# Kernel optimization log

Hardware: AMD Instinct MI355X
Metric: run time of the kernel (lower is better)

## Reference

```python
import jax, jax.numpy as jnp
import numpy as np
from jax.scipy.special import digamma

# Dims (see init_kwargs): pose P=4 -> D=16, stem A=128, primary caps B=32,
# classes C=10, class-caps kernel K=6 (== primary feature map size), 3 routing iters.
P, D, A, B, C, K, ITER = 4, 16, 128, 32, 10, 6, 3
N = B * K * K                                    # input capsules routed to each class capsule
ALPHA0, KAPPA0, NU0 = 1.0, 1.0, float(D + 1)     # Dirichlet/Normal-Wishart priors (m0=0, Psi0=I, cov='diag')
BN_EPS, EPS = 1e-5, 1e-8


def conv2d(x, w, s):
    return jax.lax.conv_general_dilated(x, w, (s, s), 'VALID',
                                        dimension_numbers=('NCHW', 'OIHW', 'NCHW'))


def bn(x, gamma, beta, axes):
    # batch-norm with batch statistics (training-mode math)
    mu = x.mean(axes, keepdims=True)
    var = x.var(axes, keepdims=True)
    return (x - mu) * jax.lax.rsqrt(var + BN_EPS) * gamma + beta


def setup_inputs():
    key = jax.random.key(0)
    ks = jax.random.split(key, 4)
    f32 = jnp.float32
    x = jax.random.normal(ks[0], (128, 3, 32, 32), dtype=f32)
    conv1_w = jax.random.normal(ks[1], (A, 3, 5, 5), dtype=f32) * 0.1
    bn1_g = jnp.ones((A,), f32); bn1_b = jnp.zeros((A,), f32)
    prim_w = jax.random.normal(ks[2], (B * D + B, A, 3, 3), dtype=f32) * 0.05
    bna_g = jnp.ones((B,), f32); bna_b = jnp.zeros((B,), f32)
    bnp_g = jnp.ones((B,), f32); bnp_b = jnp.zeros((B,), f32)
    W_ij = jax.random.normal(ks[3], (B, C, K, K, P, P), dtype=f32) * 0.3
    return dict(x=x, conv1_w=conv1_w, bn1_g=bn1_g, bn1_b=bn1_b, prim_w=prim_w,
                bna_g=bna_g, bna_b=bna_b, bnp_g=bnp_g, bnp_b=bnp_b, W_ij=W_ij)


def _vb_stats(Ra, V):
    # Ra: (b,N,C) responsibility * input activation; V: (b,N,C,D) votes
    Nj = Ra.sum(1) + EPS                                         # (b,C)
    xbar = jnp.einsum('bnc,bncd->bcd', Ra, V) / Nj[..., None]    # weighted vote mean
    diff = V - xbar[:, None]
    sigma = jnp.einsum('bnc,bncd->bcd', Ra, diff * diff) / Nj[..., None]  # diag cov
    kappa = KAPPA0 + Nj
    m = Nj[..., None] * xbar / kappa[..., None]                  # posterior mean (m0 = 0)
    nu = NU0 + Nj
    Psi = 1.0 + Nj[..., None] * sigma + (KAPPA0 * Nj / kappa)[..., None] * xbar * xbar  # Psi0 = I (diag)
    return Nj, kappa, m, nu, Psi


def _expectations(Nj, nu, Psi, d_idx):
    alpha = ALPHA0 + Nj
    E_lnpi = digamma(alpha) - digamma(alpha.sum(-1, keepdims=True))
    E_lnLam = (digamma(0.5 * (nu[..., None] + 1.0 - d_idx)).sum(-1)
               + D * jnp.log(2.0) - jnp.log(Psi).sum(-1))
    return E_lnpi, E_lnLam


def reference(x, conv1_w, bn1_g, bn1_b, prim_w, bna_g, bna_b, bnp_g, bnp_b, W_ij):
    b = x.shape[0]
    # --- stem: Conv5x5/s2 + BN + ReLU ---
    h = conv2d(x, conv1_w, 2)                                    # (b,A,14,14)
    h = jax.nn.relu(bn(h, bn1_g[None, :, None, None], bn1_b[None, :, None, None], (0, 2, 3)))
    # --- primary capsules: Conv3x3/s2 -> poses + activations ---
    pc = conv2d(h, prim_w, 2)                                    # (b,B*D+B,6,6)
    poses, a = pc[:, :B * D], pc[:, B * D:]
    a = jax.nn.sigmoid(bn(a, bna_g[None, :, None, None], bna_b[None, :, None, None], (0, 2, 3)))
    poses = bn(poses.reshape(b, B, D, K, K),
               bnp_g[None, :, None, None, None], bnp_b[None, :, None, None, None], (0, 2, 3, 4))
    poses = poses.reshape(b, B, P, P, K, K)
    # --- class capsules: votes V = W_ij @ pose, kernel covers whole 6x6 map ---
    V = jnp.einsum('icxypq,biqrxy->bicxypr', W_ij, poses)        # (b,B,C,K,K,P,P)
    V = V.transpose(0, 1, 3, 4, 2, 5, 6).reshape(b, N, C, D)
    a_i = a.reshape(b, N)
    # --- variational Bayes routing (diag Normal-Wishart, ITER iterations) ---
    d_idx = jnp.arange(1, D + 1, dtype=x.dtype)
    R = jnp.full((b, N, C), 1.0 / C, dtype=x.dtype)
    for t in range(ITER):
        Nj, kappa, m, nu, Psi = _vb_stats(R * a_i[:, :, None], V)
        if t < ITER - 1:
            E_lnpi, E_lnLam = _expectations(Nj, nu, Psi, d_idx)
            dm = V - m[:, None]
            quad = D / kappa[:, None, :] + nu[:, None, :] * jnp.einsum('bncd,bcd->bnc', dm * dm, 1.0 / Psi)
            lnp = (E_lnpi[:, None] + 0.5 * E_lnLam[:, None]
                   - 0.5 * D * jnp.log(2.0 * jnp.pi) - 0.5 * quad)
            R = jax.nn.softmax(lnp, axis=-1)
    E_lnpi, E_lnLam = _expectations(Nj, nu, Psi, d_idx)
    logits = E_lnpi + 0.5 * E_lnLam                              # (b,C)
    yhat = jax.nn.sigmoid(bn(logits, 1.0, 0.0, (0,)))            # BatchNorm1d(affine=False)
    return yhat
```

## Files before the change

### kernel.cpp

```cpp
#include <hip/hip_runtime.h>
#include <hip/hip_bf16.h>

#define NB 128
#define AA 128
#define BB 32
#define CC 10
#define KK 6
#define DD 16
#define NN 1152
#define H1 14
#define CH2 544
#define NG 4608
#define KG 1152
#define MG 576

typedef short bfrag8 __attribute__((ext_vector_type(8)));
typedef float facc4 __attribute__((ext_vector_type(4)));

__device__ __forceinline__ unsigned short f2bf(float f) {
    unsigned u = __float_as_uint(f);
    u += 0x7FFF + ((u >> 16) & 1);
    return (unsigned short)(u >> 16);
}
__device__ __forceinline__ float bf2f(unsigned short s) {
    return __uint_as_float(((unsigned)s) << 16);
}

__global__ __launch_bounds__(256, 3) void k_conv1(const float* __restrict__ x,
                                                  const float* __restrict__ w,
                                                  float* __restrict__ h) {
    __shared__ __align__(16) float sX[3][7][32];
    __shared__ float sWf[AA * 75];
    const int p = blockIdx.x;
    const int b = blockIdx.y;
    const int tid = threadIdx.x;
    for (int j = tid; j < AA * 75; j += 256) sWf[j] = w[j];
    for (int j = tid; j < 3 * 7 * 32; j += 256) {
        int col = j & 31; int t2 = j >> 5; int row = t2 % 7; int ic = t2 / 7;
        sX[ic][row][col] = x[b * 3072 + ic * 1024 + (4 * p + row) * 32 + col];
    }
    __syncthreads();
    const int oc = tid & 127, ry = tid >> 7;
    const int r = 2 * p + ry;
    float acc[14];
#pragma unroll
    for (int j = 0; j < 14; ++j) acc[j] = 0.f;
    const float* wr = sWf + oc * 75;
#pragma unroll
    for (int ic = 0; ic < 3; ++ic) {
#pragma unroll
        for (int ky = 0; ky < 5; ++ky) {
            const float* xr = &sX[ic][2 * ry + ky][0];
            float row[32];
#pragma unroll
            for (int q = 0; q < 8; ++q) {
                float4 v = *reinterpret_cast<const float4*>(xr + q * 4);
                row[q * 4 + 0] = v.x; row[q * 4 + 1] = v.y;
                row[q * 4 + 2] = v.z; row[q * 4 + 3] = v.w;
            }
            float w0 = wr[ic * 25 + ky * 5 + 0];
            float w1 = wr[ic * 25 + ky * 5 + 1];
            float w2 = wr[ic * 25 + ky * 5 + 2];
            float w3 = wr[ic * 25 + ky * 5 + 3];
            float w4 = wr[ic * 25 + ky * 5 + 4];
#pragma unroll
            for (int ox = 0; ox < 14; ++ox) {
                float s = acc[ox];
                s = fmaf(row[2 * ox + 0], w0, s);
                s = fmaf(row[2 * ox + 1], w1, s);
                s = fmaf(row[2 * ox + 2], w2, s);
                s = fmaf(row[2 * ox + 3], w3, s);
                s = fmaf(row[2 * ox + 4], w4, s);
                acc[ox] = s;
            }
        }
    }
    float* out = h + ((size_t)(b * AA + oc) * 14 + r) * 14;
#pragma unroll
    for (int q = 0; q < 7; ++q)
        *reinterpret_cast<float2*>(out + q * 2) = make_float2(acc[q * 2], acc[q * 2 + 1]);
}

__device__ __forceinline__ void blk_reduce2(float& s, float& s2, int tid) {
#pragma unroll
    for (int o = 32; o > 0; o >>= 1) { s += __shfl_down(s, o); s2 += __shfl_down(s2, o); }
    __shared__ float ls[4], lq[4];
    int lane = tid & 63, wid = tid >> 6;
    if (lane == 0) { ls[wid] = s; lq[wid] = s2; }
    __syncthreads();
    if (tid == 0) {
        s = ls[0] + ls[1] + ls[2] + ls[3];
        s2 = lq[0] + lq[1] + lq[2] + lq[3];
    }
}

__global__ void k_bnstats1a(const float* __restrict__ h, float* __restrict__ part) {
    int c = blockIdx.x & 127, sl = blockIdx.x >> 7;
    int tid = threadIdx.x;
    float s = 0.f, s2 = 0.f;
    for (int j = tid; j < 16 * 196; j += 256) {
        int b = sl * 16 + j / 196, hw = j % 196;
        float v = h[((size_t)b * AA + c) * 196 + hw];
        s += v; s2 += v * v;
    }
    blk_reduce2(s, s2, tid);
    if (tid == 0) { part[c * 8 + sl] = s; part[1024 + c * 8 + sl] = s2; }
}

__global__ void k_pim(const float* __restrict__ w, const float* __restrict__ h,
                      const float* __restrict__ part1,
                      const float* __restrict__ bn1_g, const float* __restrict__ bn1_b,
                      unsigned short* __restrict__ Ah, unsigned short* __restrict__ Al,
                      unsigned short* __restrict__ Bh, unsigned short* __restrict__ Bl) {
    const int blk = blockIdx.x;
    const int tid = threadIdx.x;
    if (blk < 324) {
        int t = blk * 256 + tid;
        int row = t / (KG / 8), seg = t % (KG / 8);
        alignas(16) unsigned short hi[8], lo[8];
        if (row < CH2) {
            const float* src = w + (size_t)row * KG + seg * 8;
#pragma unroll
            for (int j = 0; j < 8; ++j) {
                float v = src[j];
                unsigned short hh = f2bf(v);
                hi[j] = hh;
                lo[j] = f2bf(v - bf2f(hh));
            }
        } else {
#pragma unroll
            for (int j = 0; j < 8; ++j) { hi[j] = 0; lo[j] = 0; }
        }
        *reinterpret_cast<uint4*>(Ah + (size_t)row * KG + seg * 8) = *reinterpret_cast<const uint4*>(hi);
        *reinterpret_cast<uint4*>(Al + (size_t)row * KG + seg * 8) = *reinterpret_cast<const uint4*>(lo);
        return;
    }
    __shared__ float sBn1[2 * AA];
    if (tid < AA) {
        int c = tid;
        float s = 0.f, s2 = 0.f;
#pragma unroll
        for (int sl = 0; sl < 8; ++sl) { s += part1[c * 8 + sl]; s2 += part1[1024 + c * 8 + sl]; }
        const float n = (float)(NB * 196);
        float mu = s / n;
        float var = s2 / n - mu * mu;
        float sc = bn1_g[c] * rsqrtf(var + 1e-5f);
        sBn1[c] = sc;
        sBn1[AA + c] = bn1_b[c] - mu * sc;
    }
    __syncthreads();
    int t = (blk - 324) * 256 + tid;
    int n = t / (KG / 8), seg = t % (KG / 8);
    int b = n / 36, xy = n % 36;
    int oy = xy / 6, ox = xy % 6;
    const float* hb = h + (size_t)b * (AA * 196) + (2 * oy) * 14 + 2 * ox;
    alignas(16) unsigned short hi[8], lo[8];
#pragma unroll
    for (int j = 0; j < 8; ++j) {
        int k = seg * 8 + j;
        int ic = k / 9, kk = k - ic * 9;
        int ky = kk / 3, kx = kk - ky * 3;
        float v = hb[ic * 196 + ky * 14 + kx];
        v = fmaxf(fmaf(v, sBn1[ic], sBn1[AA + ic]), 0.f);
        unsigned short hh = f2bf(v);
        hi[j] = hh;
        lo[j] = f2bf(v - bf2f(hh));
    }
    *reinterpret_cast<uint4*>(Bh + (size_t)n * KG + seg * 8) = *reinterpret_cast<const uint4*>(hi);
    *reinterpret_cast<uint4*>(Bl + (size_t)n * KG + seg * 8) = *reinterpret_cast<const uint4*>(lo);
}

__global__ __launch_bounds__(256, 4) void k_gemm(const unsigned short* __restrict__ Ah,
                                                 const unsigned short* __restrict__ Al,
                                                 const unsigned short* __restrict__ Bh,
                                                 const unsigned short* __restrict__ Bl,
                                                 float* __restrict__ pcT) {
    __shared__ alignas(16) unsigned short sAh[64][44], sAl[64][44];
    __shared__ alignas(16) unsigned short sBh[64][44], sBl[64][44];
    const int s = blockIdx.x;
    const int k8 = s & 7, j = s >> 3;
    const int jm = j / 9;
    const int y = k8 + 8 * jm;
    const int xg = j - 9 * jm;
    const int oc0 = xg * 64;
    const int n0 = y * 64;
    const int tid = threadIdx.x;
    const int lane = tid & 63, wv = tid >> 6;
    const int wm = wv >> 1, wn = wv & 1;
    const int quad = lane >> 4, r16 = lane & 15;
    const int srow = tid >> 2, sseg = tid & 3;

    facc4 acc[2][2] = {};
    const size_t gA = (size_t)(oc0 + srow) * KG + sseg * 8;
    const size_t gB = (size_t)(n0 + srow) * KG + sseg * 8;

    uint4 vAh = *reinterpret_cast<const uint4*>(Ah + gA);
    uint4 vAl = *reinterpret_cast<const uint4*>(Al + gA);
    uint4 vBh = *reinterpret_cast<const uint4*>(Bh + gB);
    uint4 vBl = *reinterpret_cast<const uint4*>(Bl + gB);

    for (int ks = 0; ks < KG / 32; ++ks) {
        __syncthreads();
        *reinterpret_cast<uint4*>(&sAh[srow][sseg * 8]) = vAh;
        *reinterpret_cast<uint4*>(&sAl[srow][sseg * 8]) = vAl;
        *reinterpret_cast<uint4*>(&sBh[srow][sseg * 8]) = vBh;
        *reinterpret_cast<uint4*>(&sBl[srow][sseg * 8]) = vBl;
        __syncthreads();
        if (ks + 1 < KG / 32) {
            const int k0n = (ks + 1) * 32;
            vAh = *reinterpret_cast<const uint4*>(Ah + gA + k0n);
            vAl = *reinterpret_cast<const uint4*>(Al + gA + k0n);
            vBh = *reinterpret_cast<const uint4*>(Bh + gB + k0n);
            vBl = *reinterpret_cast<const uint4*>(Bl + gB + k0n);
        }
        bfrag8 ah[2], al[2], bh[2], bl[2];
#pragma unroll
        for (int i = 0; i < 2; ++i) {
            ah[i] = *reinterpret_cast<const bfrag8*>(&sAh[wm * 32 + i * 16 + r16][quad * 8]);
            al[i] = *reinterpret_cast<const bfrag8*>(&sAl[wm * 32 + i * 16 + r16][quad * 8]);
            bh[i] = *reinterpret_cast<const bfrag8*>(&sBh[wn * 32 + i * 16 + r16][quad * 8]);
            bl[i] = *reinterpret_cast<const bfrag8*>(&sBl[wn * 32 + i * 16 + r16][quad * 8]);
        }
#pragma unroll
        for (int i = 0; i < 2; ++i)
#pragma unroll
            for (int jj = 0; jj < 2; ++jj) {
                acc[i][jj] = __builtin_amdgcn_mfma_f32_16x16x32_bf16(ah[i], bh[jj], acc[i][jj], 0, 0, 0);
                acc[i][jj] = __builtin_amdgcn_mfma_f32_16x16x32_bf16(ah[i], bl[jj], acc[i][jj], 0, 0, 0);
                acc[i][jj] = __builtin_amdgcn_mfma_f32_16x16x32_bf16(al[i], bh[jj], acc[i][jj], 0, 0, 0);
            }
    }
#pragma unroll
    for (int i = 0; i < 2; ++i) {
        int oc_base = oc0 + wm * 32 + i * 16 + quad * 4;
        if (oc_base >= CH2) continue;
#pragma unroll
        for (int jj = 0; jj < 2; ++jj) {
            int n = n0 + wn * 32 + jj * 16 + r16;
            *reinterpret_cast<facc4*>(pcT + (size_t)n * CH2 + oc_base) = acc[i][jj];
        }
    }
}

__global__ void k_bnstats2a(const float* __restrict__ pcT, float* __restrict__ part) {
    int blk = blockIdx.x, tid = threadIdx.x;
    float s = 0.f, s2 = 0.f;
    if (blk < 256) {
        int i = blk >> 3, sl = blk & 7;
        for (int j = tid; j < 576 * 4; j += 256) {
            int row = sl * 576 + (j >> 2), q = j & 3;
            float4 v = *reinterpret_cast<const float4*>(pcT + (size_t)row * CH2 + i * 16 + q * 4);
            s += v.x + v.y + v.z + v.w;
            s2 += v.x * v.x + v.y * v.y + v.z * v.z + v.w * v.w;
        }
        blk_reduce2(s, s2, tid);
        if (tid == 0) { part[blk] = s; part[256 + blk] = s2; }
    } else {
        int t2 = blk - 256;
        int ch = t2 >> 1, sl = t2 & 1;
        for (int j = tid; j < 2304; j += 256) {
            int row = sl * 2304 + j;
            float v = pcT[(size_t)row * CH2 + BB * DD + ch];
            s += v; s2 += v * v;
        }
        blk_reduce2(s, s2, tid);
        if (tid == 0) { part[512 + t2] = s; part[576 + t2] = s2; }
    }
}

__device__ __forceinline__ float digammaf_(float x) {
    float r = 0.f;
    while (x < 6.f) { r -= 1.f / x; x += 1.f; }
    float xi = 1.f / x;
    float xi2 = xi * xi;
    return r + logf(x) - 0.5f * xi -
           xi2 * (0.0833333333f - xi2 * (0.0083333333f - xi2 * 0.0039682540f));
}

template <int FIRST>
__global__ __launch_bounds__(640) void k_routed(
    const float* __restrict__ pcT, const float* __restrict__ part2,
    const float* __restrict__ bna_g, const float* __restrict__ bna_b,
    const float* __restrict__ bnp_g, const float* __restrict__ bnp_b,
    const float* __restrict__ Wij,
    const float* __restrict__ S0i, const float* __restrict__ S1i, const float* __restrict__ S2i,
    float* __restrict__ S0o, float* __restrict__ S1o, float* __restrict__ S2o) {
    const int b = blockIdx.x >> 1, half = blockIdx.x & 1;
    const int tid = threadIdx.x;
    const int c = tid >> 6, lane = tid & 63;
    __shared__ float sLnp[CC][66];
    __shared__ float sBn2[128];
    __shared__ __align__(16) float sP[64][20];
    __shared__ float sA[64];
    __shared__ float sM[CC][16], sGq[CC][16], sBase[CC];
    if (tid < 64) {
        if (tid < 32) {
            float s = 0.f, s2 = 0.f;
#pragma unroll
            for (int sl = 0; sl < 8; ++sl) { s += part2[tid * 8 + sl]; s2 += part2[256 + tid * 8 + sl]; }
            const float n = (float)(NB * DD * 36);
            float mu = s / n, var = s2 / n - mu * mu;
            float sc = bnp_g[tid] * rsqrtf(var + 1e-5f);
            sBn2[tid] = sc; sBn2[32 + tid] = bnp_b[tid] - mu * sc;
        } else {
            int ch = tid - 32;
            float s = part2[512 + ch * 2] + part2[512 + ch * 2 + 1];
            float s2 = part2[576 + ch * 2] + part2[576 + ch * 2 + 1];
            const float n = (float)(NB * 36);
            float mu = s / n, var = s2 / n - mu * mu;
            float sc = bna_g[ch] * rsqrtf(var + 1e-5f);
            sBn2[64 + ch] = sc; sBn2[96 + ch] = bna_b[ch] - mu * sc;
        }
    }
    if (!FIRST && tid < 160) {
        int cc = tid >> 4, d = tid & 15;
        int bc = b * CC + cc;
        float njraw = S0i[bc] + S0i[NB * CC + bc];
        float nj = njraw + 1e-8f;
        float kappa = 1.f + nj;
        float nu = 17.f + nj;
        float s1 = S1i[bc * 16 + d] + S1i[(NB * CC + bc) * 16 + d];
        float s2v = S2i[bc * 16 + d] + S2i[(NB * CC + bc) * 16 + d];
        float xbar = s1 / nj;
        float sig = (s2v - 2.f * xbar * s1 + xbar * xbar * njraw) / nj;
        float Psi = 1.f + nj * sig + (nj / kappa) * xbar * xbar;
        sM[cc][d] = nj * xbar / kappa;
        sGq[cc][d] = 0.5f * nu / Psi;
        float term = digammaf_(0.5f * (nu + 1.f - (float)(d + 1))) - logf(Psi);
#pragma unroll
        for (int o = 8; o > 0; o >>= 1) term += __shfl_down(term, o, 16);
        if (d == 0) {
            float asum = 0.f;
#pragma unroll
            for (int k = 0; k < CC; ++k)
                asum += 1.f + S0i[b * CC + k] + S0i[NB * CC + b * CC + k] + 1e-8f;
            float elnlam = 16.f * 0.69314718056f + term;
            float elnpi = digammaf_(1.f + nj) - digammaf_(asum);
            float lb = elnpi + 0.5f * elnlam;
            sBase[cc] = lb - 8.f * 1.83787706641f - 8.f / kappa;
        }
    }
    __syncthreads();
    float mc[16], Gc[16], basec = 0.f;
    if (!FIRST) {
#pragma unroll
        for (int d = 0; d < 16; ++d) { mc[d] = sM[c][d]; Gc[d] = sGq[c][d]; }
        basec = sBase[c];
    }
    float s0 = 0.f, s1[16], s2[16];
#pragma unroll
    for (int d = 0; d < 16; ++d) { s1[d] = 0.f; s2[d] = 0.f; }

#pragma unroll 1
    for (int it = 0; it < 9; ++it) {
        if (tid < 256) {
            int r = tid >> 2, q = tid & 3;
            int n = half * 576 + it * 64 + r;
            int i = n / 36, xy = n - i * 36;
            int row = b * 36 + xy;
            float4 v = *reinterpret_cast<const float4*>(pcT + (size_t)row * CH2 + i * 16 + q * 4);
            float psc = sBn2[i], psh = sBn2[32 + i];
            v.x = fmaf(v.x, psc, psh); v.y = fmaf(v.y, psc, psh);
            v.z = fmaf(v.z, psc, psh); v.w = fmaf(v.w, psc, psh);
            *reinterpret_cast<float4*>(&sP[r][q * 4]) = v;
        } else if (tid < 320) {
            int r = tid - 256;
            int n = half * 576 + it * 64 + r;
            int i = n / 36, xy = n - i * 36;
            int row = b * 36 + xy;
            float va = fmaf(pcT[(size_t)row * CH2 + BB * DD + i], sBn2[64 + i], sBn2[96 + i]);
            sA[r] = 1.f / (1.f + expf(-va));
        }
        __syncthreads();
        const int n = half * 576 + it * 64 + lane;
        const int i = n / 36, xy = n - i * 36;
        const float4* wp = reinterpret_cast<const float4*>(Wij + (((size_t)i * CC + c) * 36 + xy) * 16);
        alignas(16) float P[16], W[16];
        *reinterpret_cast<float4*>(&P[0])  = *reinterpret_cast<const float4*>(&sP[lane][0]);
        *reinterpret_cast<float4*>(&P[4])  = *reinterpret_cast<const float4*>(&sP[lane][4]);
        *reinterpret_cast<float4*>(&P[8])  = *reinterpret_cast<const float4*>(&sP[lane][8]);
        *reinterpret_cast<float4*>(&P[12]) = *reinterpret_cast<const float4*>(&sP[lane][12]);
        *reinterpret_cast<float4*>(&W[0])  = wp[0];
        *reinterpret_cast<float4*>(&W[4])  = wp[1];
        *reinterpret_cast<float4*>(&W[8])  = wp[2];
        *reinterpret_cast<float4*>(&W[12]) = wp[3];
        float V[16];
#pragma unroll
        for (int p = 0; p < 4; ++p)
#pragma unroll
            for (int r = 0; r < 4; ++r)
                V[p * 4 + r] = W[p * 4 + 0] * P[0 + r] + W[p * 4 + 1] * P[4 + r] +
                               W[p * 4 + 2] * P[8 + r] + W[p * 4 + 3] * P[12 + r];
        float av = sA[lane];
        float wgt;
        if (FIRST) {
            wgt = 0.1f * av;
            __syncthreads();
        } else {
            float q = 0.f;
#pragma unroll
            for (int d = 0; d < 16; ++d) {
                float dm = V[d] - mc[d];
                q = fmaf(dm * dm, Gc[d], q);
            }
            float lnp = basec - q;
            sLnp[c][lane] = lnp;
            __syncthreads();
            float mx = -1e30f;
#pragma unroll
            for (int cc = 0; cc < CC; ++cc) mx = fmaxf(mx, sLnp[cc][lane]);
            float ssum = 0.f;
#pragma unroll
            for (int cc = 0; cc < CC; ++cc) ssum += expf(sLnp[cc][lane] - mx);
            wgt = expf(lnp - mx) / ssum * av;
        }
        s0 += wgt;
#pragma unroll
        for (int d = 0; d < 16; ++d) {
            float wv = wgt * V[d];
            s1[d] += wv;
            s2[d] = fmaf(wv, V[d], s2[d]);
        }
    }
#pragma unroll
    for (int o = 32; o > 0; o >>= 1) {
        s0 += __shfl_down(s0, o);
#pragma unroll
        for (int k = 0; k < 16; ++k) {
            s1[k] += __shfl_down(s1[k], o);
            s2[k] += __shfl_down(s2[k], o);
        }
    }
    if (lane == 0) {
        int idx = half * (NB * CC) + b * CC + c;
        S0o[idx] = s0;
#pragma unroll
        for (int k = 0; k < 16; ++k) { S1o[idx * 16 + k] = s1[k]; S2o[idx * 16 + k] = s2[k]; }
    }
}

__global__ void k_expect_final(const float* __restrict__ S0p, const float* __restrict__ S1p,
                               const float* __restrict__ S2p, float* __restrict__ logits) {
    int b = blockIdx.x;
    int c = threadIdx.x;
    __shared__ float alph[CC];
    float njraw = 0.f;
    if (c < CC) {
        njraw = S0p[b * CC + c] + S0p[NB * CC + b * CC + c];
        alph[c] = 1.f + njraw + 1e-8f;
    }
    __syncthreads();
    if (c < CC) {
        int bc = b * CC + c;
        float nj = njraw + 1e-8f;
        float asum = 0.f;
#pragma unroll
        for (int k = 0; k < CC; ++k) asum += alph[k];
        float kappa = 1.f + nj;
        float nu = 17.f + nj;
        float S0 = njraw;
        float elnlam = 16.f * 0.69314718056f;
        for (int d = 0; d < 16; ++d) {
            float s1 = S1p[bc * 16 + d] + S1p[(NB * CC + bc) * 16 + d];
            float s2v = S2p[bc * 16 + d] + S2p[(NB * CC + bc) * 16 + d];
            float xbar = s1 / nj;
            float sig = (s2v - 2.f * xbar * s1 + xbar * xbar * S0) / nj;
            float Psi = 1.f + nj * sig + (nj / kappa) * xbar * xbar;
            elnlam += digammaf_(0.5f * (nu + 1.f - (float)(d + 1))) - logf(Psi);
        }
        float elnpi = digammaf_(1.f + nj) - digammaf_(asum);
        logits[bc] = elnpi + 0.5f * elnlam;
    }
}

__global__ void k_final(const float* __restrict__ logits, float* __restrict__ out) {
    int c = blockIdx.x;
    int b = threadIdx.x;
    float v = logits[b * CC + c];
    float s = v, s2 = v * v;
#pragma unroll
    for (int o = 32; o > 0; o >>= 1) { s += __shfl_down(s, o); s2 += __shfl_down(s2, o); }
    __shared__ float ls[2], lq[2];
    int lane = b & 63, wid = b >> 6;
    if (lane == 0) { ls[wid] = s; lq[wid] = s2; }
    __syncthreads();
    float mu = (ls[0] + ls[1]) * (1.f / 128.f);
    float var = (lq[0] + lq[1]) * (1.f / 128.f) - mu * mu;
    out[b * CC + c] = 1.f / (1.f + expf(-(v - mu) * rsqrtf(var + 1e-5f)));
}

extern "C" void kernel_launch(void* const* d_in, const int* in_sizes, int n_in,
                              void* d_out, int out_size, void* d_ws, size_t ws_size,
                              hipStream_t stream) {
    (void)in_sizes; (void)n_in; (void)out_size; (void)ws_size;
    const float* x       = (const float*)d_in[0];
    const float* conv1_w = (const float*)d_in[1];
    const float* bn1_g   = (const float*)d_in[2];
    const float* bn1_b   = (const float*)d_in[3];
    const float* prim_w  = (const float*)d_in[4];
    const float* bna_g   = (const float*)d_in[5];
    const float* bna_b   = (const float*)d_in[6];
    const float* bnp_g   = (const float*)d_in[7];
    const float* bnp_b   = (const float*)d_in[8];
    const float* Wij     = (const float*)d_in[9];

    float* ws = (float*)d_ws;
    float* h   = ws;
    float* pcT = ws + 3211264;
    unsigned short* Bh = (unsigned short*)(ws + 5718016);
    unsigned short* Bl = (unsigned short*)(ws + 8372224);
    unsigned short* Ahp = (unsigned short*)(ws + 11026432);
    unsigned short* Alp = (unsigned short*)(ws + 11358208);
    float* S0a    = ws + 11690368;
    float* S1a    = ws + 11692928;
    float* S2a    = ws + 11733888;
    float* S0b    = ws + 11774848;
    float* S1b    = ws + 11777408;
    float* S2b    = ws + 11818368;
    float* logits = ws + 11859328;
    float* part1  = ws + 11860608;
    float* part2  = ws + 11862656;
    float* out    = (float*)d_out;

    k_conv1<<<dim3(7, 128), 256, 0, stream>>>(x, conv1_w, h);
    k_bnstats1a<<<1024, 256, 0, stream>>>(h, part1);
    k_pim<<<2916, 256, 0, stream>>>(prim_w, h, part1, bn1_g, bn1_b, Ahp, Alp, Bh, Bl);
    k_gemm<<<648, 256, 0, stream>>>(Ahp, Alp, Bh, Bl, pcT);
    k_bnstats2a<<<320, 256, 0, stream>>>(pcT, part2);

    k_routed<1><<<256, 640, 0, stream>>>(pcT, part2, bna_g, bna_b, bnp_g, bnp_b, Wij,
                                         S0a, S1a, S2a, S0a, S1a, S2a);
    k_routed<0><<<256, 640, 0, stream>>>(pcT, part2, bna_g, bna_b, bnp_g, bnp_b, Wij,
                                         S0a, S1a, S2a, S0b, S1b, S2b);
    k_routed<0><<<256, 640, 0, stream>>>(pcT, part2, bna_g, bna_b, bnp_g, bnp_b, Wij,
                                         S0b, S1b, S2b, S0a, S1a, S2a);
    k_expect_final<<<128, 64, 0, stream>>>(S0a, S1a, S2a, logits);

    k_final<<<10, 128, 0, stream>>>(logits, out);
}
```

Baseline: 178.2 us.

## Fuse batch-norm statistics into conv1 and GEMM epilogues, merge final kernels

Conv1 now emits per-block channel sums and sums of squares, and a small reduction kernel turns them into BN1 scale and shift. This replaces a separate full pass over the conv1 output. The GEMM epilogue computes the BN2 partial statistics from its accumulators, which removes the separate stats kernel that re-read pcT. The expectation and final sigmoid kernels are merged into one. Together this removes two launches and about two full re-reads of intermediates, at the cost of extra shuffles and syncs in the epilogues and more partial-sum entries for the routed kernel to reduce.

```diff
diff --git a/kernel.cpp b/kernel.cpp
--- a/kernel.cpp
+++ b/kernel.cpp
@@ -28,9 +28,12 @@
 
 __global__ __launch_bounds__(256, 3) void k_conv1(const float* __restrict__ x,
                                                   const float* __restrict__ w,
-                                                  float* __restrict__ h) {
+                                                  float* __restrict__ h,
+                                                  float* __restrict__ part1s,
+                                                  float* __restrict__ part1q) {
     __shared__ __align__(16) float sX[3][7][32];
     __shared__ float sWf[AA * 75];
+    __shared__ float sS[128], sQ[128];
     const int p = blockIdx.x;
     const int b = blockIdx.y;
     const int tid = threadIdx.x;
@@ -79,6 +82,16 @@
 #pragma unroll
     for (int q = 0; q < 7; ++q)
         *reinterpret_cast<float2*>(out + q * 2) = make_float2(acc[q * 2], acc[q * 2 + 1]);
+    float s_th = 0.f, q_th = 0.f;
+#pragma unroll
+    for (int ox = 0; ox < 14; ++ox) { s_th += acc[ox]; q_th = fmaf(acc[ox], acc[ox], q_th); }
+    if (ry == 1) { sS[oc] = s_th; sQ[oc] = q_th; }
+    __syncthreads();
+    if (ry == 0) {
+        int blk = p * 128 + b;
+        part1s[oc * 896 + blk] = s_th + sS[oc];
+        part1q[oc * 896 + blk] = q_th + sQ[oc];
+    }
 }
 
 __device__ __forceinline__ void blk_reduce2(float& s, float& s2, int tid) {
@@ -94,22 +107,26 @@
     }
 }
 
-__global__ void k_bnstats1a(const float* __restrict__ h, float* __restrict__ part) {
-    int c = blockIdx.x & 127, sl = blockIdx.x >> 7;
+__global__ void k_bnred1(const float* __restrict__ part1s, const float* __restrict__ part1q,
+                         const float* __restrict__ g, const float* __restrict__ be,
+                         float* __restrict__ bn1) {
+    int c = blockIdx.x;
     int tid = threadIdx.x;
     float s = 0.f, s2 = 0.f;
-    for (int j = tid; j < 16 * 196; j += 256) {
-        int b = sl * 16 + j / 196, hw = j % 196;
-        float v = h[((size_t)b * AA + c) * 196 + hw];
-        s += v; s2 += v * v;
-    }
+    for (int j = tid; j < 896; j += 256) { s += part1s[c * 896 + j]; s2 += part1q[c * 896 + j]; }
     blk_reduce2(s, s2, tid);
-    if (tid == 0) { part[c * 8 + sl] = s; part[1024 + c * 8 + sl] = s2; }
+    if (tid == 0) {
+        const float n = (float)(NB * 196);
+        float mu = s / n;
+        float var = s2 / n - mu * mu;
+        float sc = g[c] * rsqrtf(var + 1e-5f);
+        bn1[c] = sc;
+        bn1[AA + c] = be[c] - mu * sc;
+    }
 }
 
 __global__ void k_pim(const float* __restrict__ w, const float* __restrict__ h,
-                      const float* __restrict__ part1,
-                      const float* __restrict__ bn1_g, const float* __restrict__ bn1_b,
+                      const float* __restrict__ bn1,
                       unsigned short* __restrict__ Ah, unsigned short* __restrict__ Al,
                       unsigned short* __restrict__ Bh, unsigned short* __restrict__ Bl) {
     const int blk = blockIdx.x;
@@ -136,18 +153,7 @@
         return;
     }
     __shared__ float sBn1[2 * AA];
-    if (tid < AA) {
-        int c = tid;
-        float s = 0.f, s2 = 0.f;
-#pragma unroll
-        for (int sl = 0; sl < 8; ++sl) { s += part1[c * 8 + sl]; s2 += part1[1024 + c * 8 + sl]; }
-        const float n = (float)(NB * 196);
-        float mu = s / n;
-        float var = s2 / n - mu * mu;
-        float sc = bn1_g[c] * rsqrtf(var + 1e-5f);
-        sBn1[c] = sc;
-        sBn1[AA + c] = bn1_b[c] - mu * sc;
-    }
+    sBn1[tid] = bn1[tid];
     __syncthreads();
     int t = (blk - 324) * 256 + tid;
     int n = t / (KG / 8), seg = t % (KG / 8);
@@ -174,9 +180,11 @@
                                                  const unsigned short* __restrict__ Al,
                                                  const unsigned short* __restrict__ Bh,
                                                  const unsigned short* __restrict__ Bl,
-                                                 float* __restrict__ pcT) {
+                                                 float* __restrict__ pcT,
+                                                 float* __restrict__ part2) {
     __shared__ alignas(16) unsigned short sAh[64][44], sAl[64][44];
     __shared__ alignas(16) unsigned short sBh[64][44], sBl[64][44];
+    __shared__ float sRed[128];
     const int s = blockIdx.x;
     const int k8 = s & 7, j = s >> 3;
     const int jm = j / 9;
@@ -240,31 +248,63 @@
             *reinterpret_cast<facc4*>(pcT + (size_t)n * CH2 + oc_base) = acc[i][jj];
         }
     }
-}
-
-__global__ void k_bnstats2a(const float* __restrict__ pcT, float* __restrict__ part) {
-    int blk = blockIdx.x, tid = threadIdx.x;
-    float s = 0.f, s2 = 0.f;
-    if (blk < 256) {
-        int i = blk >> 3, sl = blk & 7;
-        for (int j = tid; j < 576 * 4; j += 256) {
-            int row = sl * 576 + (j >> 2), q = j & 3;
-            float4 v = *reinterpret_cast<const float4*>(pcT + (size_t)row * CH2 + i * 16 + q * 4);
-            s += v.x + v.y + v.z + v.w;
-            s2 += v.x * v.x + v.y * v.y + v.z * v.z + v.w * v.w;
-        }
-        blk_reduce2(s, s2, tid);
-        if (tid == 0) { part[blk] = s; part[256 + blk] = s2; }
+    if (xg < 8) {
+        float ps[2], pq[2];
+#pragma unroll
+        for (int i = 0; i < 2; ++i) {
+            float sv = 0.f, qv = 0.f;
+#pragma unroll
+            for (int jj = 0; jj < 2; ++jj)
+#pragma unroll
+                for (int comp = 0; comp < 4; ++comp) {
+                    float v = acc[i][jj][comp];
+                    sv += v; qv = fmaf(v, v, qv);
+                }
+#pragma unroll
+            for (int o = 32; o > 0; o >>= 1) { sv += __shfl_down(sv, o); qv += __shfl_down(qv, o); }
+            ps[i] = sv; pq[i] = qv;
+        }
+        if (lane == 0) {
+#pragma unroll
+            for (int i = 0; i < 2; ++i) { sRed[wv * 4 + i * 2 + 0] = ps[i]; sRed[wv * 4 + i * 2 + 1] = pq[i]; }
+        }
+        __syncthreads();
+        if (tid < 8) {
+            int wm_ = tid >> 2, i_ = (tid >> 1) & 1, sel = tid & 1;
+            float v = sRed[(2 * wm_) * 4 + i_ * 2 + sel] + sRed[(2 * wm_ + 1) * 4 + i_ * 2 + sel];
+            int g = xg * 4 + wm_ * 2 + i_;
+            part2[sel * 2304 + g * 72 + y] = v;
+        }
     } else {
-        int t2 = blk - 256;
-        int ch = t2 >> 1, sl = t2 & 1;
-        for (int j = tid; j < 2304; j += 256) {
-            int row = sl * 2304 + j;
-            float v = pcT[(size_t)row * CH2 + BB * DD + ch];
-            s += v; s2 += v * v;
-        }
-        blk_reduce2(s, s2, tid);
-        if (tid == 0) { part[512 + t2] = s; part[576 + t2] = s2; }
+        if (wm == 0) {
+#pragma unroll
+            for (int i = 0; i < 2; ++i)
+#pragma unroll
+                for (int comp = 0; comp < 4; ++comp) {
+                    float v0 = acc[i][0][comp], v1 = acc[i][1][comp];
+                    float sv = v0 + v1;
+                    float qv = fmaf(v0, v0, v1 * v1);
+#pragma unroll
+                    for (int o = 8; o > 0; o >>= 1) {
+                        sv += __shfl_down(sv, o, 16);
+                        qv += __shfl_down(qv, o, 16);
+                    }
+                    if (r16 == 0) {
+                        int idx = ((wv * 4 + quad) * 2 + i) * 4 + comp;
+                        sRed[idx] = sv;
+                        sRed[64 + idx] = qv;
+                    }
+                }
+        }
+        __syncthreads();
+        if (tid < 64) {
+            int ch = tid >> 1, sel = tid & 1;
+            int i_ = ch >> 4, rem = ch & 15, quad_ = rem >> 2, comp_ = rem & 3;
+            int base = sel * 64;
+            float v = sRed[base + ((0 * 4 + quad_) * 2 + i_) * 4 + comp_] +
+                      sRed[base + ((1 * 4 + quad_) * 2 + i_) * 4 + comp_];
+            part2[4608 + sel * 2304 + ch * 72 + y] = v;
+        }
     }
 }
 
@@ -295,17 +335,17 @@
     __shared__ float sM[CC][16], sGq[CC][16], sBase[CC];
     if (tid < 64) {
         if (tid < 32) {
+            int i = tid;
             float s = 0.f, s2 = 0.f;
-#pragma unroll
-            for (int sl = 0; sl < 8; ++sl) { s += part2[tid * 8 + sl]; s2 += part2[256 + tid * 8 + sl]; }
+            for (int yy = 0; yy < 72; ++yy) { s += part2[i * 72 + yy]; s2 += part2[2304 + i * 72 + yy]; }
             const float n = (float)(NB * DD * 36);
             float mu = s / n, var = s2 / n - mu * mu;
-            float sc = bnp_g[tid] * rsqrtf(var + 1e-5f);
-            sBn2[tid] = sc; sBn2[32 + tid] = bnp_b[tid] - mu * sc;
+            float sc = bnp_g[i] * rsqrtf(var + 1e-5f);
+            sBn2[i] = sc; sBn2[32 + i] = bnp_b[i] - mu * sc;
         } else {
             int ch = tid - 32;
-            float s = part2[512 + ch * 2] + part2[512 + ch * 2 + 1];
-            float s2 = part2[576 + ch * 2] + part2[576 + ch * 2 + 1];
+            float s = 0.f, s2 = 0.f;
+            for (int yy = 0; yy < 72; ++yy) { s += part2[4608 + ch * 72 + yy]; s2 += part2[6912 + ch * 72 + yy]; }
             const float n = (float)(NB * 36);
             float mu = s / n, var = s2 / n - mu * mu;
             float sc = bna_g[ch] * rsqrtf(var + 1e-5f);
@@ -439,44 +479,30 @@
     }
 }
 
-__global__ void k_expect_final(const float* __restrict__ S0p, const float* __restrict__ S1p,
-                               const float* __restrict__ S2p, float* __restrict__ logits) {
-    int b = blockIdx.x;
-    int c = threadIdx.x;
-    __shared__ float alph[CC];
-    float njraw = 0.f;
-    if (c < CC) {
-        njraw = S0p[b * CC + c] + S0p[NB * CC + b * CC + c];
-        alph[c] = 1.f + njraw + 1e-8f;
-    }
-    __syncthreads();
-    if (c < CC) {
-        int bc = b * CC + c;
-        float nj = njraw + 1e-8f;
-        float asum = 0.f;
-#pragma unroll
-        for (int k = 0; k < CC; ++k) asum += alph[k];
-        float kappa = 1.f + nj;
-        float nu = 17.f + nj;
-        float S0 = njraw;
-        float elnlam = 16.f * 0.69314718056f;
-        for (int d = 0; d < 16; ++d) {
-            float s1 = S1p[bc * 16 + d] + S1p[(NB * CC + bc) * 16 + d];
-            float s2v = S2p[bc * 16 + d] + S2p[(NB * CC + bc) * 16 + d];
-            float xbar = s1 / nj;
-            float sig = (s2v - 2.f * xbar * s1 + xbar * xbar * S0) / nj;
-            float Psi = 1.f + nj * sig + (nj / kappa) * xbar * xbar;
-            elnlam += digammaf_(0.5f * (nu + 1.f - (float)(d + 1))) - logf(Psi);
-        }
-        float elnpi = digammaf_(1.f + nj) - digammaf_(asum);
-        logits[bc] = elnpi + 0.5f * elnlam;
-    }
-}
-
-__global__ void k_final(const float* __restrict__ logits, float* __restrict__ out) {
+__global__ void k_final2(const float* __restrict__ S0p, const float* __restrict__ S1p,
+                         const float* __restrict__ S2p, float* __restrict__ out) {
     int c = blockIdx.x;
     int b = threadIdx.x;
-    float v = logits[b * CC + c];
+    int bc = b * CC + c;
+    float njraw = S0p[bc] + S0p[NB * CC + bc];
+    float nj = njraw + 1e-8f;
+    float asum = 0.f;
+#pragma unroll
+    for (int k = 0; k < CC; ++k)
+        asum += 1.f + S0p[b * CC + k] + S0p[NB * CC + b * CC + k] + 1e-8f;
+    float kappa = 1.f + nj;
+    float nu = 17.f + nj;
+    float elnlam = 16.f * 0.69314718056f;
+    for (int d = 0; d < 16; ++d) {
+        float s1 = S1p[bc * 16 + d] + S1p[(NB * CC + bc) * 16 + d];
+        float s2v = S2p[bc * 16 + d] + S2p[(NB * CC + bc) * 16 + d];
+        float xbar = s1 / nj;
+        float sig = (s2v - 2.f * xbar * s1 + xbar * xbar * njraw) / nj;
+        float Psi = 1.f + nj * sig + (nj / kappa) * xbar * xbar;
+        elnlam += digammaf_(0.5f * (nu + 1.f - (float)(d + 1))) - logf(Psi);
+    }
+    float elnpi = digammaf_(1.f + nj) - digammaf_(asum);
+    float v = elnpi + 0.5f * elnlam;
     float s = v, s2 = v * v;
 #pragma unroll
     for (int o = 32; o > 0; o >>= 1) { s += __shfl_down(s, o); s2 += __shfl_down(s2, o); }
@@ -511,22 +537,22 @@
     unsigned short* Bl = (unsigned short*)(ws + 8372224);
     unsigned short* Ahp = (unsigned short*)(ws + 11026432);
     unsigned short* Alp = (unsigned short*)(ws + 11358208);
+    float* bn1    = ws + 11689984;
     float* S0a    = ws + 11690368;
     float* S1a    = ws + 11692928;
     float* S2a    = ws + 11733888;
     float* S0b    = ws + 11774848;
     float* S1b    = ws + 11777408;
     float* S2b    = ws + 11818368;
-    float* logits = ws + 11859328;
-    float* part1  = ws + 11860608;
-    float* part2  = ws + 11862656;
+    float* part1s = ws + 11859328;
+    float* part1q = ws + 11974016;
+    float* part2  = ws + 12088704;
     float* out    = (float*)d_out;
 
-    k_conv1<<<dim3(7, 128), 256, 0, stream>>>(x, conv1_w, h);
-    k_bnstats1a<<<1024, 256, 0, stream>>>(h, part1);
-    k_pim<<<2916, 256, 0, stream>>>(prim_w, h, part1, bn1_g, bn1_b, Ahp, Alp, Bh, Bl);
-    k_gemm<<<648, 256, 0, stream>>>(Ahp, Alp, Bh, Bl, pcT);
-    k_bnstats2a<<<320, 256, 0, stream>>>(pcT, part2);
+    k_conv1<<<dim3(7, 128), 256, 0, stream>>>(x, conv1_w, h, part1s, part1q);
+    k_bnred1<<<128, 256, 0, stream>>>(part1s, part1q, bn1_g, bn1_b, bn1);
+    k_pim<<<2916, 256, 0, stream>>>(prim_w, h, bn1, Ahp, Alp, Bh, Bl);
+    k_gemm<<<648, 256, 0, stream>>>(Ahp, Alp, Bh, Bl, pcT, part2);
 
     k_routed<1><<<256, 640, 0, stream>>>(pcT, part2, bna_g, bna_b, bnp_g, bnp_b, Wij,
                                          S0a, S1a, S2a, S0a, S1a, S2a);
@@ -534,7 +560,5 @@
                                          S0a, S1a, S2a, S0b, S1b, S2b);
     k_routed<0><<<256, 640, 0, stream>>>(pcT, part2, bna_g, bna_b, bnp_g, bnp_b, Wij,
                                          S0b, S1b, S2b, S0a, S1a, S2a);
-    k_expect_final<<<128, 64, 0, stream>>>(S0a, S1a, S2a, logits);
-
-    k_final<<<10, 128, 0, stream>>>(logits, out);
-}
+    k_final2<<<10, 128, 0, stream>>>(S0a, S1a, S2a, out);
+}
```

New measurement: 186.4 us. 1.05x slower.
